# Kernel optimization log

Measured on AMD Instinct MI355X. Metric: run time of the kernel, lower is better.

## Reference

```python
import jax, jax.numpy as jnp
import numpy as np

N_NODES = 50000
N_EDGES = 800000
HIDDEN = 128
POS = 16
LAYERS = 8
HEADS = 8
HEAD_DIM = HIDDEN // HEADS
OUT = 10
N_GRAPHS = 128


def setup_inputs() -> dict:
    key = jax.random.key(0)
    ks = jax.random.split(key, 16)
    s = 1.0 / np.sqrt(HIDDEN)
    inp = {
        "X": jax.random.normal(ks[0], (N_NODES, HIDDEN), jnp.float32),
        "pos_enc": jax.random.normal(ks[1], (N_NODES, POS), jnp.float32),
        "edge_row": jnp.sort(jax.random.randint(ks[2], (N_EDGES,), 0, N_NODES, jnp.int32)),
        "edge_col": jax.random.randint(ks[3], (N_EDGES,), 0, N_NODES, jnp.int32),
        "graph_ids": jnp.sort(jax.random.randint(ks[4], (N_NODES,), 0, N_GRAPHS, jnp.int32)),
        # parameters
        "Wpos": jax.random.normal(ks[5], (POS, HIDDEN), jnp.float32) / np.sqrt(POS),
        "bpos": jnp.zeros((HIDDEN,), jnp.float32),
        "Wq": jax.random.normal(ks[6], (LAYERS, HIDDEN, HIDDEN), jnp.float32) * s,
        "bq": jnp.zeros((LAYERS, HIDDEN), jnp.float32),
        "Wk": jax.random.normal(ks[7], (LAYERS, HIDDEN, HIDDEN), jnp.float32) * s,
        "bk": jnp.zeros((LAYERS, HIDDEN), jnp.float32),
        "Wv": jax.random.normal(ks[8], (LAYERS, HIDDEN, HIDDEN), jnp.float32) * s,
        "bv": jnp.zeros((LAYERS, HIDDEN), jnp.float32),
        "Wpred": jax.random.normal(ks[9], (HIDDEN, OUT), jnp.float32) * s,
        "bpred": jnp.zeros((OUT,), jnp.float32),
    }
    return inp


def _sparse_mha(h, row, col, Wq, bq, Wk, bk, Wv, bv):
    # one SparseMHA layer: per-head SDDMM scores on edges, edge softmax per
    # destination (row of sparse A), SpMM aggregation.
    N = h.shape[0]
    scale = HEAD_DIM ** -0.5
    q = ((h @ Wq + bq).reshape(N, HEADS, HEAD_DIM)) * scale
    k = (h @ Wk + bk).reshape(N, HEADS, HEAD_DIM)
    v = (h @ Wv + bv).reshape(N, HEADS, HEAD_DIM)
    score = jnp.einsum("ehd,ehd->eh", q[row], k[col])            # [E,H]
    m = jax.ops.segment_max(score, row, num_segments=N)           # [N,H]
    ex = jnp.exp(score - m[row])
    denom = jax.ops.segment_sum(ex, row, num_segments=N)          # [N,H]
    attn = ex / denom[row]                                        # [E,H]
    out = jax.ops.segment_sum(attn[:, :, None] * v[col], row, num_segments=N)
    return out.reshape(N, HIDDEN)


def reference(X, pos_enc, edge_row, edge_col, graph_ids,
              Wpos, bpos, Wq, bq, Wk, bk, Wv, bv, Wpred, bpred):
    h = pos_enc @ Wpos + bpos                                     # [N, HIDDEN]

    def step(h, p):
        wq, bq_, wk, bk_, wv, bv_ = p
        return _sparse_mha(h, edge_row, edge_col, wq, bq_, wk, bk_, wv, bv_), None

    h, _ = jax.lax.scan(step, h, (Wq, bq, Wk, bk, Wv, bv))
    pooled = jax.ops.segment_sum(h, graph_ids, num_segments=N_GRAPHS)  # [G, HIDDEN]
    return pooled @ Wpred + bpred                                  # [G, OUT]
```

## Files before the change

kernel.cpp:

```cpp
#include <hip/hip_runtime.h>
#include <hip/hip_bf16.h>
#include <math.h>

#define N_NODES 50000
#define N_PADR  50048
#define N_EDGES 800000
#define HIDDEN  128
#define POS_DIM 16
#define LAYERS  8
#define HEADS   8
#define HEAD_DIM 16
#define OUT_DIM 10
#define N_GRAPHS 128

using f32x4 = __attribute__((ext_vector_type(4))) float;
using half8 = __attribute__((ext_vector_type(8))) _Float16;
typedef _Float16 h2 __attribute__((ext_vector_type(2)));

#if defined(__has_builtin)
#if __has_builtin(__builtin_amdgcn_fdot2)
#define HAVE_FDOT2 1
#endif
#endif

__device__ __forceinline__ unsigned packh2(float a, float b) {
    union { h2 h; unsigned u; } t;
    t.h = (h2){(_Float16)a, (_Float16)b};
    return t.u;
}
__device__ __forceinline__ float dot8(uint4 k, const unsigned* q, float s) {
#if defined(HAVE_FDOT2)
    union { unsigned u; h2 h; } a, b;
    a.u = k.x; b.u = q[0]; s = __builtin_amdgcn_fdot2(a.h, b.h, s, false);
    a.u = k.y; b.u = q[1]; s = __builtin_amdgcn_fdot2(a.h, b.h, s, false);
    a.u = k.z; b.u = q[2]; s = __builtin_amdgcn_fdot2(a.h, b.h, s, false);
    a.u = k.w; b.u = q[3]; s = __builtin_amdgcn_fdot2(a.h, b.h, s, false);
    return s;
#else
    union { unsigned u; h2 h; } a, b;
#pragma unroll
    for (int j = 0; j < 4; ++j) {
        a.u = (&k.x)[j]; b.u = q[j];
        s += (float)a.h[0] * (float)b.h[0] + (float)a.h[1] * (float)b.h[1];
    }
    return s;
#endif
}

__global__ void k_row_ptr(const int* __restrict__ row, int* __restrict__ row_ptr) {
    int e = blockIdx.x * blockDim.x + threadIdx.x;
    if (e >= N_EDGES) return;
    int cur  = row[e];
    int prev = (e == 0) ? -1 : row[e - 1];
    for (int r = prev + 1; r <= cur; ++r) row_ptr[r] = e;
    if (e == N_EDGES - 1) {
        for (int r = cur + 1; r <= N_NODES; ++r) row_ptr[r] = N_EDGES;
    }
}

__global__ __launch_bounds__(256) void k_wprep(const float* __restrict__ Wq,
                                               const float* __restrict__ Wk,
                                               const float* __restrict__ Wv,
                                               unsigned short* __restrict__ Wt) {
    __shared__ float sT[32][33];
    const int l3 = blockIdx.x >> 4, tile = blockIdx.x & 15;
    const int layer = l3 / 3, mat = l3 % 3;
    const float* src = (mat == 0 ? Wq : mat == 1 ? Wk : Wv) + (size_t)layer * HIDDEN * HIDDEN;
    unsigned short* dh = Wt + (size_t)l3 * HIDDEN * HIDDEN;
    const int k0 = (tile >> 2) * 32, n0 = (tile & 3) * 32;
    const int tx = threadIdx.x & 31, ty = threadIdx.x >> 5;
#pragma unroll
    for (int i = 0; i < 4; ++i)
        sT[ty + i * 8][tx] = src[(size_t)(k0 + ty + i * 8) * HIDDEN + n0 + tx];
    __syncthreads();
#pragma unroll
    for (int i = 0; i < 4; ++i) {
        const int nr = ty + i * 8;
        union { h2 h; unsigned u; } t;
        t.h = (h2){(_Float16)sT[tx][nr], (_Float16)0.f};
        dh[(size_t)(n0 + nr) * HIDDEN + k0 + tx] = (unsigned short)(t.u & 0xffffu);
    }
}

__global__ __launch_bounds__(256) void k_pos(const float* __restrict__ pos,
                                             const float* __restrict__ Wpos,
                                             const float* __restrict__ bpos,
                                             unsigned short* __restrict__ h) {
    __shared__ float sW[POS_DIM][HIDDEN];
    __shared__ float sb[HIDDEN];
    int t = threadIdx.x;
    for (int i = t; i < POS_DIM * HIDDEN; i += 256) sW[i / HIDDEN][i % HIDDEN] = Wpos[i];
    if (t < HIDDEN) sb[t] = bpos[t];
    __syncthreads();
    int n = blockIdx.x * 2 + (t >> 7);
    int j = t & 127;
    if (n >= N_NODES) return;
    float acc = sb[j];
#pragma unroll
    for (int q = 0; q < POS_DIM; ++q) acc += pos[n * POS_DIM + q] * sW[q][j];
    union { h2 h; unsigned u; } v;
    v.h = (h2){(_Float16)acc, (_Float16)0.f};
    h[(size_t)n * HIDDEN + j] = (unsigned short)(v.u & 0xffffu);
}

__global__ __launch_bounds__(256, 2) void k_qkv(const unsigned short* __restrict__ h,
                                                const unsigned short* __restrict__ Wt,
                                                const float* __restrict__ bq,
                                                const float* __restrict__ bk,
                                                const float* __restrict__ bv,
                                                unsigned* __restrict__ Qh,
                                                unsigned short* __restrict__ KV,
                                                int layer) {
    __shared__ unsigned char sA[64 * 256];

    const int t = threadIdx.x;
    const int w = t >> 6, lane = t & 63;
    const int c = lane >> 4, r = lane & 15;
    const int m0 = blockIdx.x * 64;

    {
        const char* src = (const char*)h + (size_t)m0 * 256;
        const int s_base = w * 256;
#pragma unroll
        for (int i = 0; i < 4; ++i) {
            const int s   = s_base + i * 64 + lane;
            const int row = s >> 4;
            const int ch  = s & 15;
            const char* g = src + row * 256 + ((ch ^ (row & 15)) << 4);
            char* l = (char*)&sA[(s_base + i * 64) << 4];
            __builtin_amdgcn_global_load_lds(
                (const __attribute__((address_space(1))) unsigned int*)g,
                (__attribute__((address_space(3))) unsigned int*)l, 16, 0, 0);
        }
    }
    __syncthreads();

    const int nbase = w * 2;

#pragma unroll 1
    for (int mat = 0; mat < 3; ++mat) {
        const unsigned short* wt = Wt + (size_t)(layer * 3 + mat) * (HIDDEN * HIDDEN);
        half8 B[2][4];
#pragma unroll
        for (int nbp = 0; nbp < 2; ++nbp)
#pragma unroll
            for (int kc = 0; kc < 4; ++kc)
                B[nbp][kc] = *(const half8*)&wt[(size_t)((nbase + nbp) * 16 + r) * HIDDEN + kc * 32 + c * 8];

        f32x4 acc[4][2];
#pragma unroll
        for (int mb = 0; mb < 4; ++mb)
#pragma unroll
            for (int nbp = 0; nbp < 2; ++nbp)
                acc[mb][nbp] = (f32x4){0.f, 0.f, 0.f, 0.f};

#pragma unroll
        for (int mb = 0; mb < 4; ++mb) {
            const int lr = mb * 16 + r;
            half8 a[4];
#pragma unroll
            for (int kc = 0; kc < 4; ++kc) {
                const int chunk = ((kc << 2) + c) ^ (lr & 15);
                a[kc] = *(const half8*)&sA[lr * 256 + (chunk << 4)];
            }
#pragma unroll
            for (int nbp = 0; nbp < 2; ++nbp)
#pragma unroll
                for (int kc = 0; kc < 4; ++kc)
                    acc[mb][nbp] = __builtin_amdgcn_mfma_f32_16x16x32_f16(B[nbp][kc], a[kc], acc[mb][nbp], 0, 0, 0);
        }

        const float* bias = (mat == 0 ? bq : mat == 1 ? bk : bv) + layer * HIDDEN;
#pragma unroll
        for (int mb = 0; mb < 4; ++mb) {
            const size_t m = m0 + mb * 16 + r;
#pragma unroll
            for (int nbp = 0; nbp < 2; ++nbp) {
                const int n0 = (nbase + nbp) * 16 + c * 4;
                float4 b4 = *(const float4*)&bias[n0];
                float v0 = acc[mb][nbp][0] + b4.x;
                float v1 = acc[mb][nbp][1] + b4.y;
                float v2 = acc[mb][nbp][2] + b4.z;
                float v3 = acc[mb][nbp][3] + b4.w;
                if (mat == 0) {
                    uint2 o = make_uint2(packh2(v0 * 0.25f, v1 * 0.25f),
                                         packh2(v2 * 0.25f, v3 * 0.25f));
                    *(uint2*)&Qh[m * 64 + (n0 >> 1)] = o;
                } else {
                    uint2 o = make_uint2(packh2(v0, v1), packh2(v2, v3));
                    unsigned short* dst = KV + m * 256 + (mat == 2 ? 128 : 0) + n0;
                    *(uint2*)dst = o;
                }
            }
        }
    }
}

__global__ __launch_bounds__(256) void k_attn(const unsigned* __restrict__ Qh,
                                              const unsigned short* __restrict__ KV,
                                              const int* __restrict__ col,
                                              const int* __restrict__ row_ptr,
                                              unsigned short* __restrict__ hout) {
    int wid  = (blockIdx.x * blockDim.x + threadIdx.x) >> 6;
    int lane = threadIdx.x & 63;
    if (wid >= N_NODES) return;
    const int g  = lane >> 3;
    const int lg = lane & 7;
    const int d0 = lg * 16;
    const int start = row_ptr[wid];
    const int end   = row_ptr[wid + 1];

    unsigned q2[8];
    {
        uint4 qa = *(const uint4*)&Qh[(size_t)wid * 64 + lg * 8];
        uint4 qb = *(const uint4*)&Qh[(size_t)wid * 64 + lg * 8 + 4];
        q2[0] = qa.x; q2[1] = qa.y; q2[2] = qa.z; q2[3] = qa.w;
        q2[4] = qb.x; q2[5] = qb.y; q2[6] = qb.z; q2[7] = qb.w;
    }

    float dsum = 0.f;
    float acc[16];
#pragma unroll
    for (int i = 0; i < 16; ++i) acc[i] = 0.f;

    int e = start + g;
    int c = (e < end) ? col[e] : -1;
    uint4 kA, kB, vA, vB;
    if (c >= 0) {
        const uint4* kp = (const uint4*)(KV + (size_t)c * 256 + d0);
        const uint4* vp = (const uint4*)(KV + (size_t)c * 256 + 128 + d0);
        kA = kp[0]; kB = kp[1]; vA = vp[0]; vB = vp[1];
    }
    while (c >= 0) {
        int en = e + 8;
        int cn = (en < end) ? col[en] : -1;
        uint4 nkA, nkB, nvA, nvB;
        if (cn >= 0) {
            const uint4* kp = (const uint4*)(KV + (size_t)cn * 256 + d0);
            const uint4* vp = (const uint4*)(KV + (size_t)cn * 256 + 128 + d0);
            nkA = kp[0]; nkB = kp[1]; nvA = vp[0]; nvB = vp[1];
        }
        float s = dot8(kA, q2, 0.f);
        s = dot8(kB, q2 + 4, s);
        float p = __expf(s);
        dsum += p;
        union { unsigned u; h2 h; } tv;
#pragma unroll
        for (int j = 0; j < 4; ++j) {
            tv.u = (&vA.x)[j];
            acc[2 * j]     += p * (float)tv.h[0];
            acc[2 * j + 1] += p * (float)tv.h[1];
        }
#pragma unroll
        for (int j = 0; j < 4; ++j) {
            tv.u = (&vB.x)[j];
            acc[8 + 2 * j]     += p * (float)tv.h[0];
            acc[8 + 2 * j + 1] += p * (float)tv.h[1];
        }
        e = en; c = cn;
        kA = nkA; kB = nkB; vA = nvA; vB = nvB;
    }
#pragma unroll
    for (int off = 8; off < 64; off <<= 1) {
        dsum += __shfl_xor(dsum, off);
#pragma unroll
        for (int i = 0; i < 16; ++i) acc[i] += __shfl_xor(acc[i], off);
    }
    if (g == 0) {
        float inv = (end > start) ? 1.f / fmaxf(dsum, 1e-30f) : 0.f;
        unsigned hw[8];
#pragma unroll
        for (int j = 0; j < 8; ++j)
            hw[j] = packh2(acc[2 * j] * inv, acc[2 * j + 1] * inv);
        uint4* ph = (uint4*)(hout + (size_t)wid * HIDDEN + d0);
        ph[0] = make_uint4(hw[0], hw[1], hw[2], hw[3]);
        ph[1] = make_uint4(hw[4], hw[5], hw[6], hw[7]);
    }
}

__global__ __launch_bounds__(256) void k_pool(const unsigned short* __restrict__ h,
                                              const int* __restrict__ gid,
                                              float* __restrict__ pooled) {
    const int ch   = threadIdx.x & 127;
    const int half = threadIdx.x >> 7;
    const int n0   = blockIdx.x * 128 + half * 64;
    float run = 0.f;
    int   rg  = -1;
    for (int i = 0; i < 64; ++i) {
        int n = n0 + i;
        if (n >= N_NODES) break;
        int g = gid[n];
        if (g != rg) {
            if (rg >= 0) atomicAdd(&pooled[rg * HIDDEN + ch], run);
            rg = g; run = 0.f;
        }
        union { unsigned u; h2 hh; } v;
        v.u = (unsigned)h[(size_t)n * HIDDEN + ch];
        run += (float)v.hh[0];
    }
    if (rg >= 0) atomicAdd(&pooled[rg * HIDDEN + ch], run);
}

__global__ void k_pred(const float* __restrict__ pooled, const float* __restrict__ Wp,
                       const float* __restrict__ bp, float* __restrict__ out) {
    int idx = blockIdx.x * blockDim.x + threadIdx.x;
    if (idx >= N_GRAPHS * OUT_DIM) return;
    int g = idx / OUT_DIM, o = idx % OUT_DIM;
    float acc = bp[o];
#pragma unroll 4
    for (int j = 0; j < HIDDEN; ++j) acc += pooled[g * HIDDEN + j] * Wp[j * OUT_DIM + o];
    out[idx] = acc;
}

extern "C" void kernel_launch(void* const* d_in, const int* in_sizes, int n_in,
                              void* d_out, int out_size, void* d_ws, size_t ws_size,
                              hipStream_t stream) {
    const float* pos   = (const float*)d_in[1];
    const int*   erow  = (const int*)d_in[2];
    const int*   ecol  = (const int*)d_in[3];
    const int*   gid   = (const int*)d_in[4];
    const float* Wpos  = (const float*)d_in[5];
    const float* bpos  = (const float*)d_in[6];
    const float* Wq    = (const float*)d_in[7];
    const float* bq    = (const float*)d_in[8];
    const float* Wk    = (const float*)d_in[9];
    const float* bk    = (const float*)d_in[10];
    const float* Wv    = (const float*)d_in[11];
    const float* bv    = (const float*)d_in[12];
    const float* Wpred = (const float*)d_in[13];
    const float* bpred = (const float*)d_in[14];
    float* out = (float*)d_out;

    char* base = (char*)d_ws;
    size_t off = 0;
    auto alloc = [&](size_t bytes) {
        void* r = base + off;
        off += (bytes + 255) & ~(size_t)255;
        return r;
    };
    unsigned short* h    = (unsigned short*)alloc((size_t)N_PADR * HIDDEN * 2);
    unsigned*       Qh   = (unsigned*)alloc((size_t)N_PADR * 64 * 4);
    unsigned short* KVb  = (unsigned short*)alloc((size_t)N_PADR * 256 * 2);
    unsigned short* Wt   = (unsigned short*)alloc((size_t)LAYERS * 3 * HIDDEN * HIDDEN * 2);
    int*   rowp   = (int*)alloc((size_t)(N_NODES + 1) * 4);
    float* pooled = (float*)alloc((size_t)N_GRAPHS * HIDDEN * 4);

    k_row_ptr<<<(N_EDGES + 255) / 256, 256, 0, stream>>>(erow, rowp);
    k_wprep<<<LAYERS * 3 * 16, 256, 0, stream>>>(Wq, Wk, Wv, Wt);
    k_pos<<<N_NODES / 2, 256, 0, stream>>>(pos, Wpos, bpos, h);

    for (int l = 0; l < LAYERS; ++l) {
        k_qkv<<<N_PADR / 64, 256, 0, stream>>>(h, Wt, bq, bk, bv, Qh, KVb, l);
        k_attn<<<(N_NODES * 64 + 255) / 256, 256, 0, stream>>>(Qh, KVb, ecol, rowp, h);
    }

    hipMemsetAsync(pooled, 0, N_GRAPHS * HIDDEN * 4, stream);
    k_pool<<<(N_NODES + 127) / 128, 256, 0, stream>>>(h, gid, pooled);
    k_pred<<<(N_GRAPHS * OUT_DIM + 255) / 256, 256, 0, stream>>>(pooled, Wpred, bpred, out);
}
```

Baseline: 822.9 us.

## Retile QKV GEMM to 128-row blocks with double-buffered weight fragments

The QKV projection kernel now processes 128 rows per block with 512 threads. Each wave owns one 16-column slice and iterates over 8 row sub-blocks. The B weight fragments for the next matrix are prefetched while the current one is computed. The Q scaling factor is folded into the prepared fp16 weights and the bias, which removes a per-output multiply. Together these aim to improve weight reuse and latency hiding in exchange for more LDS per block and different occupancy.

```diff
diff --git a/kernel.cpp b/kernel.cpp
--- a/kernel.cpp
+++ b/kernel.cpp
@@ -66,6 +66,7 @@
     const int l3 = blockIdx.x >> 4, tile = blockIdx.x & 15;
     const int layer = l3 / 3, mat = l3 % 3;
     const float* src = (mat == 0 ? Wq : mat == 1 ? Wk : Wv) + (size_t)layer * HIDDEN * HIDDEN;
+    const float scl = (mat == 0) ? 0.25f : 1.0f;
     unsigned short* dh = Wt + (size_t)l3 * HIDDEN * HIDDEN;
     const int k0 = (tile >> 2) * 32, n0 = (tile & 3) * 32;
     const int tx = threadIdx.x & 31, ty = threadIdx.x >> 5;
@@ -77,7 +78,7 @@
     for (int i = 0; i < 4; ++i) {
         const int nr = ty + i * 8;
         union { h2 h; unsigned u; } t;
-        t.h = (h2){(_Float16)sT[tx][nr], (_Float16)0.f};
+        t.h = (h2){(_Float16)(sT[tx][nr] * scl), (_Float16)0.f};
         dh[(size_t)(n0 + nr) * HIDDEN + k0 + tx] = (unsigned short)(t.u & 0xffffu);
     }
 }
@@ -103,7 +104,7 @@
     h[(size_t)n * HIDDEN + j] = (unsigned short)(v.u & 0xffffu);
 }
 
-__global__ __launch_bounds__(256, 2) void k_qkv(const unsigned short* __restrict__ h,
+__global__ __launch_bounds__(512, 4) void k_qkv(const unsigned short* __restrict__ h,
                                                 const unsigned short* __restrict__ Wt,
                                                 const float* __restrict__ bq,
                                                 const float* __restrict__ bk,
@@ -111,86 +112,82 @@
                                                 unsigned* __restrict__ Qh,
                                                 unsigned short* __restrict__ KV,
                                                 int layer) {
-    __shared__ unsigned char sA[64 * 256];
+    __shared__ unsigned char sA[128 * 256];
 
     const int t = threadIdx.x;
     const int w = t >> 6, lane = t & 63;
     const int c = lane >> 4, r = lane & 15;
-    const int m0 = blockIdx.x * 64;
+    const int m0 = blockIdx.x * 128;
 
     {
         const char* src = (const char*)h + (size_t)m0 * 256;
-        const int s_base = w * 256;
 #pragma unroll
         for (int i = 0; i < 4; ++i) {
-            const int s   = s_base + i * 64 + lane;
+            const int s   = i * 512 + t;
             const int row = s >> 4;
             const int ch  = s & 15;
             const char* g = src + row * 256 + ((ch ^ (row & 15)) << 4);
-            char* l = (char*)&sA[(s_base + i * 64) << 4];
+            char* l = (char*)&sA[s << 4];
             __builtin_amdgcn_global_load_lds(
                 (const __attribute__((address_space(1))) unsigned int*)g,
                 (__attribute__((address_space(3))) unsigned int*)l, 16, 0, 0);
         }
     }
+
+    int aoff[4];
+#pragma unroll
+    for (int kc = 0; kc < 4; ++kc) aoff[kc] = ((((kc << 2) + c) ^ r) << 4);
+
+    const size_t wrow = (size_t)(w * 16 + r) * HIDDEN + c * 8;
+    const unsigned short* wt0 = Wt + (size_t)(layer * 3) * (HIDDEN * HIDDEN);
+
+    half8 B[2][4];
+#pragma unroll
+    for (int kc = 0; kc < 4; ++kc)
+        B[0][kc] = *(const half8*)&wt0[wrow + kc * 32];
+
     __syncthreads();
 
-    const int nbase = w * 2;
-
-#pragma unroll 1
+#pragma unroll
     for (int mat = 0; mat < 3; ++mat) {
-        const unsigned short* wt = Wt + (size_t)(layer * 3 + mat) * (HIDDEN * HIDDEN);
-        half8 B[2][4];
-#pragma unroll
-        for (int nbp = 0; nbp < 2; ++nbp)
+        const int cur = mat & 1;
+        if (mat < 2) {
+            const unsigned short* wtn = Wt + (size_t)(layer * 3 + mat + 1) * (HIDDEN * HIDDEN);
 #pragma unroll
             for (int kc = 0; kc < 4; ++kc)
-                B[nbp][kc] = *(const half8*)&wt[(size_t)((nbase + nbp) * 16 + r) * HIDDEN + kc * 32 + c * 8];
-
-        f32x4 acc[4][2];
-#pragma unroll
-        for (int mb = 0; mb < 4; ++mb)
-#pragma unroll
-            for (int nbp = 0; nbp < 2; ++nbp)
-                acc[mb][nbp] = (f32x4){0.f, 0.f, 0.f, 0.f};
-
-#pragma unroll
-        for (int mb = 0; mb < 4; ++mb) {
-            const int lr = mb * 16 + r;
-            half8 a[4];
-#pragma unroll
-            for (int kc = 0; kc < 4; ++kc) {
-                const int chunk = ((kc << 2) + c) ^ (lr & 15);
-                a[kc] = *(const half8*)&sA[lr * 256 + (chunk << 4)];
-            }
-#pragma unroll
-            for (int nbp = 0; nbp < 2; ++nbp)
-#pragma unroll
-                for (int kc = 0; kc < 4; ++kc)
-                    acc[mb][nbp] = __builtin_amdgcn_mfma_f32_16x16x32_f16(B[nbp][kc], a[kc], acc[mb][nbp], 0, 0, 0);
+                B[cur ^ 1][kc] = *(const half8*)&wtn[wrow + kc * 32];
+        }
+
+        f32x4 acc[8];
+#pragma unroll
+        for (int mb = 0; mb < 8; ++mb) acc[mb] = (f32x4){0.f, 0.f, 0.f, 0.f};
+
+#pragma unroll
+        for (int mb = 0; mb < 8; ++mb) {
+            const int abase = (mb * 16 + r) * 256;
+            half8 a0 = *(const half8*)&sA[abase + aoff[0]];
+            half8 a1 = *(const half8*)&sA[abase + aoff[1]];
+            half8 a2 = *(const half8*)&sA[abase + aoff[2]];
+            half8 a3 = *(const half8*)&sA[abase + aoff[3]];
+            acc[mb] = __builtin_amdgcn_mfma_f32_16x16x32_f16(B[cur][0], a0, acc[mb], 0, 0, 0);
+            acc[mb] = __builtin_amdgcn_mfma_f32_16x16x32_f16(B[cur][1], a1, acc[mb], 0, 0, 0);
+            acc[mb] = __builtin_amdgcn_mfma_f32_16x16x32_f16(B[cur][2], a2, acc[mb], 0, 0, 0);
+            acc[mb] = __builtin_amdgcn_mfma_f32_16x16x32_f16(B[cur][3], a3, acc[mb], 0, 0, 0);
         }
 
         const float* bias = (mat == 0 ? bq : mat == 1 ? bk : bv) + layer * HIDDEN;
-#pragma unroll
-        for (int mb = 0; mb < 4; ++mb) {
+        float4 b4 = *(const float4*)&bias[w * 16 + c * 4];
+        if (mat == 0) { b4.x *= 0.25f; b4.y *= 0.25f; b4.z *= 0.25f; b4.w *= 0.25f; }
+#pragma unroll
+        for (int mb = 0; mb < 8; ++mb) {
             const size_t m = m0 + mb * 16 + r;
-#pragma unroll
-            for (int nbp = 0; nbp < 2; ++nbp) {
-                const int n0 = (nbase + nbp) * 16 + c * 4;
-                float4 b4 = *(const float4*)&bias[n0];
-                float v0 = acc[mb][nbp][0] + b4.x;
-                float v1 = acc[mb][nbp][1] + b4.y;
-                float v2 = acc[mb][nbp][2] + b4.z;
-                float v3 = acc[mb][nbp][3] + b4.w;
-                if (mat == 0) {
-                    uint2 o = make_uint2(packh2(v0 * 0.25f, v1 * 0.25f),
-                                         packh2(v2 * 0.25f, v3 * 0.25f));
-                    *(uint2*)&Qh[m * 64 + (n0 >> 1)] = o;
-                } else {
-                    uint2 o = make_uint2(packh2(v0, v1), packh2(v2, v3));
-                    unsigned short* dst = KV + m * 256 + (mat == 2 ? 128 : 0) + n0;
-                    *(uint2*)dst = o;
-                }
+            uint2 o = make_uint2(packh2(acc[mb][0] + b4.x, acc[mb][1] + b4.y),
+                                 packh2(acc[mb][2] + b4.z, acc[mb][3] + b4.w));
+            if (mat == 0) {
+                *(uint2*)&Qh[m * 64 + w * 8 + c * 2] = o;
+            } else {
+                unsigned short* dst = KV + m * 256 + (mat == 2 ? 128 : 0) + w * 16 + c * 4;
+                *(uint2*)dst = o;
             }
         }
     }
@@ -350,7 +347,7 @@
     k_pos<<<N_NODES / 2, 256, 0, stream>>>(pos, Wpos, bpos, h);
 
     for (int l = 0; l < LAYERS; ++l) {
-        k_qkv<<<N_PADR / 64, 256, 0, stream>>>(h, Wt, bq, bk, bv, Qh, KVb, l);
+        k_qkv<<<N_PADR / 128, 512, 0, stream>>>(h, Wt, bq, bk, bv, Qh, KVb, l);
         k_attn<<<(N_NODES * 64 + 255) / 256, 256, 0, stream>>>(Qh, KVb, ecol, rowp, h);
     }
 
```

After: 949.1 us. 15.3% more time.

## Split QKV projection across a grid dimension per matrix and fold Q scale into weights

Applied to the files above, without the earlier changes.

The QKV kernel now launches three blocks per 64-row tile (one per Q/K/V matrix) instead of looping over the three matrices inside one block, giving three times more blocks. The B-weight loads are issued before the barrier so they overlap with the async LDS fill. The 0.25 Q scaling is folded into the fp16 weights at prep time and into the bias. The cost is that each tile of h is loaded from global memory three times instead of once, and the occupancy hint was dropped from launch bounds.

```diff
diff --git a/kernel.cpp b/kernel.cpp
--- a/kernel.cpp
+++ b/kernel.cpp
@@ -66,6 +66,7 @@
     const int l3 = blockIdx.x >> 4, tile = blockIdx.x & 15;
     const int layer = l3 / 3, mat = l3 % 3;
     const float* src = (mat == 0 ? Wq : mat == 1 ? Wk : Wv) + (size_t)layer * HIDDEN * HIDDEN;
+    const float scl = (mat == 0) ? 0.25f : 1.0f;
     unsigned short* dh = Wt + (size_t)l3 * HIDDEN * HIDDEN;
     const int k0 = (tile >> 2) * 32, n0 = (tile & 3) * 32;
     const int tx = threadIdx.x & 31, ty = threadIdx.x >> 5;
@@ -77,7 +78,7 @@
     for (int i = 0; i < 4; ++i) {
         const int nr = ty + i * 8;
         union { h2 h; unsigned u; } t;
-        t.h = (h2){(_Float16)sT[tx][nr], (_Float16)0.f};
+        t.h = (h2){(_Float16)(sT[tx][nr] * scl), (_Float16)0.f};
         dh[(size_t)(n0 + nr) * HIDDEN + k0 + tx] = (unsigned short)(t.u & 0xffffu);
     }
 }
@@ -103,94 +104,95 @@
     h[(size_t)n * HIDDEN + j] = (unsigned short)(v.u & 0xffffu);
 }
 
-__global__ __launch_bounds__(256, 2) void k_qkv(const unsigned short* __restrict__ h,
-                                                const unsigned short* __restrict__ Wt,
-                                                const float* __restrict__ bq,
-                                                const float* __restrict__ bk,
-                                                const float* __restrict__ bv,
-                                                unsigned* __restrict__ Qh,
-                                                unsigned short* __restrict__ KV,
-                                                int layer) {
+__global__ __launch_bounds__(256) void k_qkv(const unsigned short* __restrict__ h,
+                                             const unsigned short* __restrict__ Wt,
+                                             const float* __restrict__ bq,
+                                             const float* __restrict__ bk,
+                                             const float* __restrict__ bv,
+                                             unsigned* __restrict__ Qh,
+                                             unsigned short* __restrict__ KV,
+                                             int layer) {
     __shared__ unsigned char sA[64 * 256];
 
     const int t = threadIdx.x;
     const int w = t >> 6, lane = t & 63;
     const int c = lane >> 4, r = lane & 15;
     const int m0 = blockIdx.x * 64;
+    const int mat = blockIdx.y;
 
     {
         const char* src = (const char*)h + (size_t)m0 * 256;
-        const int s_base = w * 256;
 #pragma unroll
         for (int i = 0; i < 4; ++i) {
-            const int s   = s_base + i * 64 + lane;
+            const int s   = i * 256 + t;
             const int row = s >> 4;
             const int ch  = s & 15;
             const char* g = src + row * 256 + ((ch ^ (row & 15)) << 4);
-            char* l = (char*)&sA[(s_base + i * 64) << 4];
+            char* l = (char*)&sA[(i * 256 + w * 64) << 4];
             __builtin_amdgcn_global_load_lds(
                 (const __attribute__((address_space(1))) unsigned int*)g,
                 (__attribute__((address_space(3))) unsigned int*)l, 16, 0, 0);
         }
     }
+
+    const unsigned short* wt = Wt + (size_t)(layer * 3 + mat) * (HIDDEN * HIDDEN);
+    const int nbase = w * 2;
+    half8 B[2][4];
+#pragma unroll
+    for (int nbp = 0; nbp < 2; ++nbp)
+#pragma unroll
+        for (int kc = 0; kc < 4; ++kc)
+            B[nbp][kc] = *(const half8*)&wt[(size_t)((nbase + nbp) * 16 + r) * HIDDEN + kc * 32 + c * 8];
+
     __syncthreads();
 
-    const int nbase = w * 2;
-
-#pragma unroll 1
-    for (int mat = 0; mat < 3; ++mat) {
-        const unsigned short* wt = Wt + (size_t)(layer * 3 + mat) * (HIDDEN * HIDDEN);
-        half8 B[2][4];
+    f32x4 acc[4][2];
+#pragma unroll
+    for (int mb = 0; mb < 4; ++mb)
 #pragma unroll
         for (int nbp = 0; nbp < 2; ++nbp)
+            acc[mb][nbp] = (f32x4){0.f, 0.f, 0.f, 0.f};
+
+#pragma unroll
+    for (int mb = 0; mb < 4; ++mb) {
+        const int abase = (mb * 16 + r) * 256;
+        half8 a[4];
+#pragma unroll
+        for (int kc = 0; kc < 4; ++kc)
+            a[kc] = *(const half8*)&sA[abase + ((((kc << 2) + c) ^ r) << 4)];
+#pragma unroll
+        for (int nbp = 0; nbp < 2; ++nbp)
 #pragma unroll
             for (int kc = 0; kc < 4; ++kc)
-                B[nbp][kc] = *(const half8*)&wt[(size_t)((nbase + nbp) * 16 + r) * HIDDEN + kc * 32 + c * 8];
-
-        f32x4 acc[4][2];
-#pragma unroll
-        for (int mb = 0; mb < 4; ++mb)
-#pragma unroll
-            for (int nbp = 0; nbp < 2; ++nbp)
-                acc[mb][nbp] = (f32x4){0.f, 0.f, 0.f, 0.f};
-
-#pragma unroll
-        for (int mb = 0; mb < 4; ++mb) {
-            const int lr = mb * 16 + r;
-            half8 a[4];
-#pragma unroll
-            for (int kc = 0; kc < 4; ++kc) {
-                const int chunk = ((kc << 2) + c) ^ (lr & 15);
-                a[kc] = *(const half8*)&sA[lr * 256 + (chunk << 4)];
+                acc[mb][nbp] = __builtin_amdgcn_mfma_f32_16x16x32_f16(B[nbp][kc], a[kc], acc[mb][nbp], 0, 0, 0);
+    }
+
+    const float* bias = (mat == 0 ? bq : mat == 1 ? bk : bv) + layer * HIDDEN;
+#pragma unroll
+    for (int mb = 0; mb < 4; ++mb) {
+        const size_t m = m0 + mb * 16 + r;
+#pragma unroll
+        for (int nbp = 0; nbp < 2; ++nbp) {
+            const int n0 = (nbase + nbp) * 16 + c * 4;
+            float4 b4 = *(const float4*)&bias[n0];
+            float v0, v1, v2, v3;
+            if (mat == 0) {
+                v0 = acc[mb][nbp][0] + b4.x * 0.25f;
+                v1 = acc[mb][nbp][1] + b4.y * 0.25f;
+                v2 = acc[mb][nbp][2] + b4.z * 0.25f;
+                v3 = acc[mb][nbp][3] + b4.w * 0.25f;
+            } else {
+                v0 = acc[mb][nbp][0] + b4.x;
+                v1 = acc[mb][nbp][1] + b4.y;
+                v2 = acc[mb][nbp][2] + b4.z;
+                v3 = acc[mb][nbp][3] + b4.w;
             }
-#pragma unroll
-            for (int nbp = 0; nbp < 2; ++nbp)
-#pragma unroll
-                for (int kc = 0; kc < 4; ++kc)
-                    acc[mb][nbp] = __builtin_amdgcn_mfma_f32_16x16x32_f16(B[nbp][kc], a[kc], acc[mb][nbp], 0, 0, 0);
-        }
-
-        const float* bias = (mat == 0 ? bq : mat == 1 ? bk : bv) + layer * HIDDEN;
-#pragma unroll
-        for (int mb = 0; mb < 4; ++mb) {
-            const size_t m = m0 + mb * 16 + r;
-#pragma unroll
-            for (int nbp = 0; nbp < 2; ++nbp) {
-                const int n0 = (nbase + nbp) * 16 + c * 4;
-                float4 b4 = *(const float4*)&bias[n0];
-                float v0 = acc[mb][nbp][0] + b4.x;
-                float v1 = acc[mb][nbp][1] + b4.y;
-                float v2 = acc[mb][nbp][2] + b4.z;
-                float v3 = acc[mb][nbp][3] + b4.w;
-                if (mat == 0) {
-                    uint2 o = make_uint2(packh2(v0 * 0.25f, v1 * 0.25f),
-                                         packh2(v2 * 0.25f, v3 * 0.25f));
-                    *(uint2*)&Qh[m * 64 + (n0 >> 1)] = o;
-                } else {
-                    uint2 o = make_uint2(packh2(v0, v1), packh2(v2, v3));
-                    unsigned short* dst = KV + m * 256 + (mat == 2 ? 128 : 0) + n0;
-                    *(uint2*)dst = o;
-                }
+            uint2 o = make_uint2(packh2(v0, v1), packh2(v2, v3));
+            if (mat == 0) {
+                *(uint2*)&Qh[m * 64 + (n0 >> 1)] = o;
+            } else {
+                unsigned short* dst = KV + m * 256 + (mat == 2 ? 128 : 0) + n0;
+                *(uint2*)dst = o;
             }
         }
     }
@@ -350,7 +352,8 @@
     k_pos<<<N_NODES / 2, 256, 0, stream>>>(pos, Wpos, bpos, h);
 
     for (int l = 0; l < LAYERS; ++l) {
-        k_qkv<<<N_PADR / 64, 256, 0, stream>>>(h, Wt, bq, bk, bv, Qh, KVb, l);
+        dim3 g(N_PADR / 64, 3, 1);
+        k_qkv<<<g, 256, 0, stream>>>(h, Wt, bq, bk, bv, Qh, KVb, l);
         k_attn<<<(N_NODES * 64 + 255) / 256, 256, 0, stream>>>(Qh, KVb, ecol, rowp, h);
     }
 
```

After: 848.0 us. 3.1% more time.
